# Performance work log

Hardware: AMD Instinct MI355X
Metric: run time of the kernel (lower is better)

Reference implementation:

```python
import jax, jax.numpy as jnp
import numpy as np

N = 50000      # nodes
E = 800000     # edges (before self loops)
F_IN = 16      # n_input_features
PRE = 32       # n_channels_preproc
C = 128        # n_channels
GH = 32        # edge_gate_hidden_dim
L = 5          # n_gnn_layers (tied weights)


def setup_inputs() -> dict:
    key = jax.random.key(0)
    ks = jax.random.split(key, 16)
    def w(k, shape):
        return jax.random.normal(k, shape, jnp.float32) * 0.05
    return dict(
        x=jax.random.normal(ks[0], (N, F_IN), jnp.float32),
        edge_index=jax.random.randint(ks[1], (2, E), 0, N),
        edge_attr=jax.random.normal(ks[2], (E, 1), jnp.float32),
        W_pre=w(ks[3], (F_IN, PRE)), b_pre=jnp.zeros((PRE,), jnp.float32),
        W_init=w(ks[4], (PRE, C)), b_init=jnp.zeros((C,), jnp.float32),
        W_g1=w(ks[5], (2 * C + 1, GH)), b_g1=jnp.zeros((GH,), jnp.float32),
        W_g2=w(ks[6], (GH, 1)), b_g2=jnp.zeros((1,), jnp.float32),
        W_z=w(ks[7], (2 * C, C)), b_z=jnp.zeros((C,), jnp.float32),
        W_r=w(ks[8], (2 * C, C)), b_r=jnp.zeros((C,), jnp.float32),
        W_h=w(ks[9], (2 * C, C)), b_h=jnp.zeros((C,), jnp.float32),
        W_f1=w(ks[10], (2 * C, C)), b_f1=jnp.zeros((C,), jnp.float32),
        W_f2=w(ks[11], (C, 2)), b_f2=jnp.zeros((2,), jnp.float32),
    )


def reference(x, edge_index, edge_attr,
              W_pre, b_pre, W_init, b_init,
              W_g1, b_g1, W_g2, b_g2,
              W_z, b_z, W_r, b_r, W_h, b_h,
              W_f1, b_f1, W_f2, b_f2):
    n = x.shape[0]
    # add self loops (fill_value=0.0 for edge_attr)
    sl = jnp.arange(n)
    row = jnp.concatenate([edge_index[0], sl])   # source (x_j)
    col = jnp.concatenate([edge_index[1], sl])   # target (x_i), aggregation index
    ea = jnp.concatenate([edge_attr, jnp.zeros((n, 1), x.dtype)], axis=0)
    # symmetric normalization from in-degree (degree of col, incl. self loops)
    deg = jax.ops.segment_sum(jnp.ones(col.shape[0], x.dtype), col, num_segments=n)
    dis = jnp.where(deg > 0, deg ** -0.5, 0.0)
    norm = (dis[row] * dis[col])[:, None]        # [E', 1]

    # preproc + initial node transform
    h = jax.nn.relu(x @ W_pre + b_pre)
    h0 = jax.nn.relu(h @ W_init + b_init)
    h = h0

    for _ in range(L):  # tied GGNN layers
        x_i = h[col]                              # gather target feats  [E', C]
        x_j = h[row]                              # gather source feats  [E', C]
        g_in = jnp.concatenate([x_i, x_j, ea], axis=-1)          # [E', 2C+1]
        gate = jax.nn.sigmoid(jax.nn.relu(g_in @ W_g1 + b_g1) @ W_g2 + b_g2)
        msg = gate * (norm * x_j)                                  # [E', C]
        aggr = jax.ops.segment_sum(msg, col, num_segments=n)       # scatter-add
        # GRU-style update
        za = jnp.concatenate([h, aggr], axis=-1)                   # [N, 2C]
        z = jax.nn.sigmoid(za @ W_z + b_z)
        r = jax.nn.sigmoid(za @ W_r + b_r)
        hc = jax.nn.relu(jnp.concatenate([r * h, aggr], axis=-1) @ W_h + b_h)
        h = (1.0 - z) * h + z * hc

    out = jnp.concatenate([h0, h], axis=-1)       # [N, 2C]
    out = jax.nn.relu(out @ W_f1 + b_f1)
    return out @ W_f2 + b_f2                      # [N, 2] logits (output_activation='none')
```

## Files before the change

### kernel.cpp

```cpp
#include <hip/hip_runtime.h>
#include <math.h>

#define NODES 50000
#define NEDGES 800000
#define ETOT (NEDGES + NODES)
#define FIN 16
#define PRE 32
#define C 128
#define GH 32
#define LAYERS 5
#define RECS 160
#define SCB 64
#define SCT 256
#define SCCH ((NODES + SCB*SCT - 1) / (SCB*SCT))

typedef _Float16 f16;
typedef f16 f16x8 __attribute__((ext_vector_type(8)));
typedef f16 f16x4 __attribute__((ext_vector_type(4)));
typedef f16 f16x2 __attribute__((ext_vector_type(2)));
typedef float f32x4 __attribute__((ext_vector_type(4)));

__device__ __forceinline__ float sigmoidf_(float x) { return 1.0f / (1.0f + __expf(-x)); }

__device__ __forceinline__ int swz_off(int row, int bytecol, int stride) {
    return row * stride + ((((bytecol) >> 4) ^ (row & 7)) << 4) + (bytecol & 15);
}
__device__ __forceinline__ int ps_off(int row, int bytecol) {
    return row * 64 + ((((bytecol) >> 4) ^ (row & 3)) << 4) + (bytecol & 15);
}

__device__ __forceinline__ int bperm(int c) { return 4 * (c & 7) + (c >> 3); }

__global__ void k_degree(const int* __restrict__ col, float* __restrict__ deg) {
    int e = blockIdx.x * blockDim.x + threadIdx.x;
    if (e < NEDGES) atomicAdd(&deg[col[e]], 1.0f);
}

__global__ __launch_bounds__(SCT) void k_scan1(const float* __restrict__ deg, int* __restrict__ bsum) {
    __shared__ int ws4[SCT / 64];
    int b = blockIdx.x, t = threadIdx.x;
    int lane = t & 63, wv = t >> 6;
    int base = (b * SCT + t) * SCCH;
    int sum = 0;
#pragma unroll
    for (int j = 0; j < SCCH; j++) {
        int i = base + j;
        if (i < NODES) sum += (int)deg[i] + 1;
    }
#pragma unroll
    for (int off = 32; off > 0; off >>= 1) sum += __shfl_xor(sum, off, 64);
    if (lane == 0) ws4[wv] = sum;
    __syncthreads();
    if (t == 0) {
        int tot = 0;
#pragma unroll
        for (int j = 0; j < SCT / 64; j++) tot += ws4[j];
        bsum[b] = tot;
    }
}

__global__ __launch_bounds__(64) void k_scan2(const int* __restrict__ bsum, int* __restrict__ bscan,
                                              int* __restrict__ start) {
    int t = threadIdx.x;
    int v = (t < SCB) ? bsum[t] : 0;
    int x = v;
#pragma unroll
    for (int off = 1; off < 64; off <<= 1) {
        int tt = __shfl_up(x, off, 64);
        if (t >= off) x += tt;
    }
    if (t < SCB) bscan[t] = x - v;
    if (t == SCB - 1) start[NODES] = x;
}

__global__ __launch_bounds__(SCT) void k_scan3(
    float* __restrict__ deg_dis, const int* __restrict__ bscan,
    int* __restrict__ start, int* __restrict__ cursor) {
    __shared__ int woff[SCT / 64];
    int b = blockIdx.x, t = threadIdx.x;
    int lane = t & 63, wv = t >> 6;
    int base = (b * SCT + t) * SCCH;
    int v[SCCH]; int sum = 0;
#pragma unroll
    for (int j = 0; j < SCCH; j++) {
        int i = base + j;
        v[j] = (i < NODES) ? (int)deg_dis[i] + 1 : 0;
        sum += v[j];
    }
    int x = sum;
#pragma unroll
    for (int off = 1; off < 64; off <<= 1) {
        int tt = __shfl_up(x, off, 64);
        if (lane >= off) x += tt;
    }
    int texcl = x - sum;
    if (lane == 63) woff[wv] = x;
    __syncthreads();
    int wbase = 0;
    for (int j = 0; j < wv; j++) wbase += woff[j];
    int run = bscan[b] + wbase + texcl;
#pragma unroll
    for (int j = 0; j < SCCH; j++) {
        int i = base + j;
        if (i < NODES) {
            start[i] = run; cursor[i] = run;
            deg_dis[i] = rsqrtf((float)v[j]);
        }
        run += v[j];
    }
}

__global__ __launch_bounds__(256) void k_csr(
    const int* __restrict__ eidx, const float* __restrict__ eattr,
    int* __restrict__ cursor,
    int* __restrict__ row_sorted, float* __restrict__ ea_sorted) {
    int e = blockIdx.x * blockDim.x + threadIdx.x;
    if (e >= ETOT) return;
    int r, ci; float ea;
    if (e < NEDGES) { r = eidx[e]; ci = eidx[NEDGES + e]; ea = eattr[e]; }
    else            { r = ci = e - NEDGES; ea = 0.0f; }
    int slot = atomicAdd(&cursor[ci], 1);
    row_sorted[slot] = r;
    ea_sorted[slot] = ea;
}

__global__ __launch_bounds__(256) void k_prep_w(
    const float* __restrict__ Wz, const float* __restrict__ Wr, const float* __restrict__ Wh,
    const float* __restrict__ Wg1, const float* __restrict__ Wf1,
    const float* __restrict__ Wpre, const float* __restrict__ Winit,
    f16* __restrict__ WcatF, f16* __restrict__ WhtopF, f16* __restrict__ Wg1F,
    f16* __restrict__ Wf1F, f16* __restrict__ WpreF, f16* __restrict__ WinitF) {
    int t = blockIdx.x * 256 + threadIdx.x;
    int l = t & 63;
    int lr = l & 15, lh = l >> 4;
    if (t < 24 * 8 * 64) {
        int idx = t >> 6; int nt = idx >> 3, ks = idx & 7;
        int wv = nt / 6, ntl = nt % 6;
        int grp = ntl >> 1, pr = ntl & 1;
        int ncol = (2 * wv + pr) * 16 + lr;
        f16x8 v;
#pragma unroll
        for (int j = 0; j < 8; j++) {
            int k = ks * 32 + lh * 8 + j;
            float x;
            if (grp == 0)      x = Wz[k * 128 + ncol];
            else if (grp == 1) x = Wr[k * 128 + ncol];
            else               x = (k >= 128) ? Wh[k * 128 + ncol] : 0.0f;
            v[j] = (f16)x;
        }
        *(f16x8*)(WcatF + (size_t)t * 8) = v;
    } else if (t < 24 * 8 * 64 + 8 * 4 * 64) {
        int t2 = t - 24 * 8 * 64;
        int idx = t2 >> 6; int nt = idx >> 2, ks = idx & 3;
        int n = nt * 16 + lr;
        f16x8 v;
#pragma unroll
        for (int j = 0; j < 8; j++) {
            int k = ks * 32 + lh * 8 + j;
            v[j] = (f16)Wh[k * 128 + n];
        }
        *(f16x8*)(WhtopF + (size_t)t2 * 8) = v;
    } else if (t < 24 * 8 * 64 + 8 * 4 * 64 + 4 * 4 * 64) {
        int t3 = t - (24 * 8 * 64 + 8 * 4 * 64);
        int idx = t3 >> 6; int nt = idx >> 2, ks = idx & 3;
        int cg = nt * 16 + lr;
        f16x8 v;
#pragma unroll
        for (int j = 0; j < 8; j++) {
            int k = ks * 32 + lh * 8 + j;
            v[j] = (f16)((cg < 32) ? Wg1[k * GH + cg] : Wg1[(128 + k) * GH + (cg - 32)]);
        }
        *(f16x8*)(Wg1F + (size_t)t3 * 8) = v;
    } else if (t < 24 * 8 * 64 + 8 * 4 * 64 + 4 * 4 * 64 + 8 * 8 * 64) {
        int t4 = t - (24 * 8 * 64 + 8 * 4 * 64 + 4 * 4 * 64);
        int idx = t4 >> 6; int nt = idx >> 3, ks = idx & 7;
        int n = nt * 16 + lr;
        f16x8 v;
#pragma unroll
        for (int j = 0; j < 8; j++) {
            int k = ks * 32 + lh * 8 + j;
            v[j] = (f16)Wf1[k * 128 + n];
        }
        *(f16x8*)(Wf1F + (size_t)t4 * 8) = v;
    } else if (t < 19456 + 2 * 64) {
        int t5 = t - 19456;
        int nt = t5 >> 6;
        f16x8 v;
#pragma unroll
        for (int j = 0; j < 8; j++) {
            int k = lh * 8 + j;
            v[j] = (k < FIN) ? (f16)Wpre[k * PRE + nt * 16 + lr] : (f16)0.0f;
        }
        *(f16x8*)(WpreF + (size_t)t5 * 8) = v;
    } else if (t < 19456 + 128 + 8 * 64) {
        int t6 = t - 19456 - 128;
        int nt = t6 >> 6;
        f16x8 v;
#pragma unroll
        for (int j = 0; j < 8; j++) {
            int k = lh * 8 + j;
            v[j] = (f16)Winit[k * C + nt * 16 + lr];
        }
        *(f16x8*)(WinitF + (size_t)t6 * 8) = v;
    }
}

__global__ __launch_bounds__(256) void k_pre_gate(
    const float* __restrict__ x, const float* __restrict__ bpre, const float* __restrict__ binit,
    const float* __restrict__ dis,
    const f16* __restrict__ WpreF, const f16* __restrict__ WinitF,
    const f16* __restrict__ Wg1F, const float* __restrict__ bg1,
    f16* __restrict__ h0_16, f16* __restrict__ h16, f16* __restrict__ rec,
    float* __restrict__ A) {
    __shared__ f16 ps[32 * 32];
    __shared__ f16 za[32 * 128];
    char* psB = (char*)ps;
    char* zaB = (char*)za;
    int tid = threadIdx.x;
    int l = tid & 63, w = tid >> 6;
    int lr = l & 15, lh = l >> 4;
    int n0 = blockIdx.x * 32;
    int rt0 = w >> 1, ct = w & 1;

    f16x8 xa = {};
    {
        int gn = n0 + rt0 * 16 + lr;
        if (gn < NODES && lh < 2) {
            float4 xv0 = *(const float4*)(x + (size_t)gn * FIN + lh * 8);
            float4 xv1 = *(const float4*)(x + (size_t)gn * FIN + lh * 8 + 4);
            xa[0] = (f16)xv0.x; xa[1] = (f16)xv0.y; xa[2] = (f16)xv0.z; xa[3] = (f16)xv0.w;
            xa[4] = (f16)xv1.x; xa[5] = (f16)xv1.y; xa[6] = (f16)xv1.z; xa[7] = (f16)xv1.w;
        }
    }
    f16x8 bA = *(const f16x8*)(WpreF + ((size_t)ct * 64 + l) * 8);
    f32x4 accA; accA[0] = accA[1] = accA[2] = accA[3] = 0.0f;
    accA = __builtin_amdgcn_mfma_f32_16x16x32_f16(xa, bA, accA, 0, 0, 0);
    {
        float bp = bpre[ct * 16 + lr];
#pragma unroll
        for (int j = 0; j < 4; j++) {
            int row = rt0 * 16 + lh * 4 + j;
            float v = fmaxf(accA[j] + bp, 0.0f);
            *(f16*)(psB + ps_off(row, (ct * 16 + lr) * 2)) = (f16)v;
        }
    }
    __syncthreads();

    f16x8 pa0 = *(const f16x8*)(psB + ps_off(lr, lh * 16));
    f16x8 pa1 = *(const f16x8*)(psB + ps_off(lr + 16, lh * 16));
    f32x4 accB[2][2];
#pragma unroll
    for (int rt = 0; rt < 2; rt++)
#pragma unroll
        for (int ntl = 0; ntl < 2; ntl++)
#pragma unroll
            for (int j = 0; j < 4; j++) accB[rt][ntl][j] = 0.0f;
#pragma unroll
    for (int ntl = 0; ntl < 2; ntl++) {
        f16x8 b = *(const f16x8*)(WinitF + ((size_t)((w * 2 + ntl) * 64 + l)) * 8);
        accB[0][ntl] = __builtin_amdgcn_mfma_f32_16x16x32_f16(pa0, b, accB[0][ntl], 0, 0, 0);
        accB[1][ntl] = __builtin_amdgcn_mfma_f32_16x16x32_f16(pa1, b, accB[1][ntl], 0, 0, 0);
    }
#pragma unroll
    for (int rt = 0; rt < 2; rt++)
#pragma unroll
        for (int ntl = 0; ntl < 2; ntl++) {
            int cg = (w * 2 + ntl) * 16 + lr;
            float bi = binit[cg];
#pragma unroll
            for (int j = 0; j < 4; j++) {
                int row = rt * 16 + lh * 4 + j;
                float v = fmaxf(accB[rt][ntl][j] + bi, 0.0f);
                *(f16*)(zaB + swz_off(row, cg * 2, 256)) = (f16)v;
            }
        }
    __syncthreads();

    for (int p = tid; p < 32 * 16; p += 256) {
        int row = p >> 4, seg = p & 15;
        int gn = n0 + row;
        if (gn < NODES) {
            f16x8 v = *(const f16x8*)(zaB + swz_off(row, seg * 16, 256));
            *(f16x8*)(h0_16 + (size_t)gn * C + seg * 8) = v;
            *(f16x8*)(h16 + (size_t)gn * C + seg * 8) = v;
            float dn = dis[gn];
            f16x8 od;
#pragma unroll
            for (int j = 0; j < 8; j++) od[j] = (f16)((float)v[j] * dn);
            *(f16x8*)(rec + (size_t)gn * RECS + 32 + seg * 8) = od;
        }
    }

    f32x4 acc3[2];
#pragma unroll
    for (int rt = 0; rt < 2; rt++)
#pragma unroll
        for (int j = 0; j < 4; j++) acc3[rt][j] = 0.0f;
#pragma unroll
    for (int ks = 0; ks < 4; ks++) {
        int kk = ks * 32 + lh * 8;
        f16x8 a0 = *(const f16x8*)(zaB + swz_off(lr,      kk * 2, 256));
        f16x8 a1 = *(const f16x8*)(zaB + swz_off(lr + 16, kk * 2, 256));
        f16x8 b = *(const f16x8*)(Wg1F + ((size_t)(w * 4 + ks) * 64 + l) * 8);
        acc3[0] = __builtin_amdgcn_mfma_f32_16x16x32_f16(a0, b, acc3[0], 0, 0, 0);
        acc3[1] = __builtin_amdgcn_mfma_f32_16x16x32_f16(a1, b, acc3[1], 0, 0, 0);
    }
    int col3 = w * 16 + lr;
#pragma unroll
    for (int rt = 0; rt < 2; rt++)
#pragma unroll
        for (int j = 0; j < 4; j++) {
            int row = rt * 16 + lh * 4 + j;
            int gn = n0 + row;
            if (gn < NODES) {
                float v = acc3[rt][j];
                if (col3 < 32) A[(size_t)gn * GH + bperm(col3)] = v + bg1[col3];
                else           rec[(size_t)gn * RECS + bperm(col3 - 32)] = (f16)v;
            }
        }
}

__global__ __launch_bounds__(256) void k_msg(
    const int* __restrict__ start, const int* __restrict__ row_sorted,
    const float* __restrict__ ea_sorted, const float* __restrict__ dis,
    const float* __restrict__ A, const f16* __restrict__ rec,
    const float* __restrict__ Wg1, const float* __restrict__ Wg2, const float* __restrict__ bg2,
    f16* __restrict__ aggr16) {
    int wid = (blockIdx.x * blockDim.x + threadIdx.x) >> 6;
    int lane = threadIdx.x & 63;
    if (wid >= NODES) return;
    int k8 = lane & 7;
    int q = lane >> 3;
    int s0 = start[wid], s1 = start[wid + 1];
    float4 a4 = *(const float4*)(A + (size_t)wid * GH + k8 * 4);
    const float* wg1e = Wg1 + 2 * C * GH;
    float wea0 = wg1e[k8], wea1 = wg1e[k8 + 8], wea2 = wg1e[k8 + 16], wea3 = wg1e[k8 + 24];
    float w20 = Wg2[k8], w21 = Wg2[k8 + 8], w22 = Wg2[k8 + 16], w23 = Wg2[k8 + 24];
    float b2 = bg2[0];
    float dci = dis[wid];
    float acc[16];
#pragma unroll
    for (int j = 0; j < 16; j++) acc[j] = 0.0f;

    int s = s0 + q;
    f16x8 ha0 = {}, hb0 = {};
    f16x4 bb0 = {};
    float ea0 = 0.0f;
    if (s < s1) {
        int r = row_sorted[s];
        ea0 = ea_sorted[s];
        const f16* rr = rec + (size_t)r * RECS;
        bb0 = *(const f16x4*)(rr + k8 * 4);
        ha0 = *(const f16x8*)(rr + 32 + k8 * 16);
        hb0 = *(const f16x8*)(rr + 32 + k8 * 16 + 8);
    }
    while (s < s1) {
        int s2 = s + 8;
        f16x8 ha1 = {}, hb1 = {};
        f16x4 bb1 = {};
        float ea1 = 0.0f;
        if (s2 < s1) {
            int r = row_sorted[s2];
            ea1 = ea_sorted[s2];
            const f16* rr = rec + (size_t)r * RECS;
            bb1 = *(const f16x4*)(rr + k8 * 4);
            ha1 = *(const f16x8*)(rr + 32 + k8 * 16);
            hb1 = *(const f16x8*)(rr + 32 + k8 * 16 + 8);
        }
        float t0 = fmaxf(a4.x + (float)bb0[0] + ea0 * wea0, 0.0f);
        float t1 = fmaxf(a4.y + (float)bb0[1] + ea0 * wea1, 0.0f);
        float t2 = fmaxf(a4.z + (float)bb0[2] + ea0 * wea2, 0.0f);
        float t3 = fmaxf(a4.w + (float)bb0[3] + ea0 * wea3, 0.0f);
        float p = t0 * w20;
        p = fmaf(t1, w21, p);
        p = fmaf(t2, w22, p);
        p = fmaf(t3, w23, p);
        p += __shfl_xor(p, 4, 8);
        p += __shfl_xor(p, 2, 8);
        p += __shfl_xor(p, 1, 8);
        float coef = sigmoidf_(p + b2);
#pragma unroll
        for (int j = 0; j < 8; j++) {
            acc[j]     = fmaf(coef, (float)ha0[j], acc[j]);
            acc[8 + j] = fmaf(coef, (float)hb0[j], acc[8 + j]);
        }
        ha0 = ha1; hb0 = hb1; bb0 = bb1; ea0 = ea1;
        s = s2;
    }
#pragma unroll
    for (int j = 0; j < 16; j++) {
        acc[j] += __shfl_xor(acc[j], 8, 64);
        acc[j] += __shfl_xor(acc[j], 16, 64);
        acc[j] += __shfl_xor(acc[j], 32, 64);
    }
    if (lane < 8) {
        f16x8 o1, o2;
#pragma unroll
        for (int j = 0; j < 8; j++) { o1[j] = (f16)(acc[j] * dci); o2[j] = (f16)(acc[8 + j] * dci); }
        *(f16x8*)(aggr16 + (size_t)wid * C + k8 * 16) = o1;
        *(f16x8*)(aggr16 + (size_t)wid * C + k8 * 16 + 8) = o2;
    }
}

__global__ __launch_bounds__(256) void k_update_mfma(
    f16* __restrict__ h16, const f16* __restrict__ aggr16, const float* __restrict__ dis,
    f16* __restrict__ rec,
    const f16* __restrict__ WcatF, const f16* __restrict__ WhtopF, const f16* __restrict__ Wg1F,
    const float* __restrict__ bz, const float* __restrict__ br, const float* __restrict__ bh,
    const float* __restrict__ bg1,
    float* __restrict__ A) {
    __shared__ f16 za[32 * 256];
    __shared__ f16 rhbuf[32 * 128];
    char* zaB = (char*)za;
    char* rhB = (char*)rhbuf;
    int tid = threadIdx.x;
    int l = tid & 63, w = tid >> 6;
    int lr = l & 15, lh = l >> 4;
    int n0 = blockIdx.x * 32;

    for (int p = tid; p < 32 * 16; p += 256) {
        int row = p >> 4, seg = p & 15;
        int gn = n0 + row;
        f16x8 v = {};
        if (gn < NODES) v = *(const f16x8*)(h16 + (size_t)gn * C + seg * 8);
        *(f16x8*)(zaB + swz_off(row, seg * 16, 512)) = v;
    }
    for (int p = tid; p < 32 * 16; p += 256) {
        int row = p >> 4, seg = p & 15;
        int gn = n0 + row;
        f16x8 v = {};
        if (gn < NODES) v = *(const f16x8*)(aggr16 + (size_t)gn * C + seg * 8);
        *(f16x8*)(zaB + swz_off(row, 256 + seg * 16, 512)) = v;
    }
    __syncthreads();

    f32x4 acc[2][6];
#pragma unroll
    for (int rt = 0; rt < 2; rt++)
#pragma unroll
        for (int n = 0; n < 6; n++)
#pragma unroll
            for (int j = 0; j < 4; j++) acc[rt][n][j] = 0.0f;
#pragma unroll
    for (int ks = 0; ks < 8; ks++) {
        int kk = ks * 32 + lh * 8;
        f16x8 a0 = *(const f16x8*)(zaB + swz_off(lr,      kk * 2, 512));
        f16x8 a1 = *(const f16x8*)(zaB + swz_off(lr + 16, kk * 2, 512));
#pragma unroll
        for (int ntl = 0; ntl < 6; ntl++) {
            f16x8 b = *(const f16x8*)(WcatF + ((size_t)((w * 6 + ntl) * 8 + ks) * 64 + l) * 8);
            acc[0][ntl] = __builtin_amdgcn_mfma_f32_16x16x32_f16(a0, b, acc[0][ntl], 0, 0, 0);
            acc[1][ntl] = __builtin_amdgcn_mfma_f32_16x16x32_f16(a1, b, acc[1][ntl], 0, 0, 0);
        }
    }

    float zreg[2][2][4];
#pragma unroll
    for (int rt = 0; rt < 2; rt++)
#pragma unroll
        for (int pr = 0; pr < 2; pr++) {
            int cg = (2 * w + pr) * 16 + lr;
#pragma unroll
            for (int j = 0; j < 4; j++) {
                int row = rt * 16 + lh * 4 + j;
                zreg[rt][pr][j] = sigmoidf_(acc[rt][pr][j] + bz[cg]);
                float rv = sigmoidf_(acc[rt][2 + pr][j] + br[cg]);
                float hv = (float)*(const f16*)(zaB + swz_off(row, cg * 2, 512));
                *(f16*)(rhB + swz_off(row, cg * 2, 256)) = (f16)(rv * hv);
            }
        }
    __syncthreads();

    f32x4 acc2[2][2];
#pragma unroll
    for (int rt = 0; rt < 2; rt++)
#pragma unroll
        for (int pr = 0; pr < 2; pr++) {
            int cg = (2 * w + pr) * 16 + lr;
#pragma unroll
            for (int j = 0; j < 4; j++)
                acc2[rt][pr][j] = acc[rt][4 + pr][j] + bh[cg];
        }
#pragma unroll
    for (int ks = 0; ks < 4; ks++) {
        int kk = ks * 32 + lh * 8;
        f16x8 a0 = *(const f16x8*)(rhB + swz_off(lr,      kk * 2, 256));
        f16x8 a1 = *(const f16x8*)(rhB + swz_off(lr + 16, kk * 2, 256));
#pragma unroll
        for (int pr = 0; pr < 2; pr++) {
            f16x8 b = *(const f16x8*)(WhtopF + ((size_t)((w * 2 + pr) * 4 + ks) * 64 + l) * 8);
            acc2[0][pr] = __builtin_amdgcn_mfma_f32_16x16x32_f16(a0, b, acc2[0][pr], 0, 0, 0);
            acc2[1][pr] = __builtin_amdgcn_mfma_f32_16x16x32_f16(a1, b, acc2[1][pr], 0, 0, 0);
        }
    }

#pragma unroll
    for (int rt = 0; rt < 2; rt++)
#pragma unroll
        for (int pr = 0; pr < 2; pr++) {
            int cg = (2 * w + pr) * 16 + lr;
#pragma unroll
            for (int j = 0; j < 4; j++) {
                int row = rt * 16 + lh * 4 + j;
                int gn = n0 + row;
                float hc = fmaxf(acc2[rt][pr][j], 0.0f);
                float z = zreg[rt][pr][j];
                float hold = (float)*(const f16*)(zaB + swz_off(row, cg * 2, 512));
                float hn = (1.0f - z) * hold + z * hc;
                if (gn < NODES) {
                    h16[(size_t)gn * C + cg] = (f16)hn;
                    rec[(size_t)gn * RECS + 32 + cg] = (f16)(hn * dis[gn]);
                }
                *(f16*)(zaB + swz_off(row, cg * 2, 512)) = (f16)hn;
            }
        }
    __syncthreads();

    f32x4 acc3[2];
#pragma unroll
    for (int rt = 0; rt < 2; rt++)
#pragma unroll
        for (int j = 0; j < 4; j++) acc3[rt][j] = 0.0f;
#pragma unroll
    for (int ks = 0; ks < 4; ks++) {
        int kk = ks * 32 + lh * 8;
        f16x8 a0 = *(const f16x8*)(zaB + swz_off(lr,      kk * 2, 512));
        f16x8 a1 = *(const f16x8*)(zaB + swz_off(lr + 16, kk * 2, 512));
        f16x8 b = *(const f16x8*)(Wg1F + ((size_t)(w * 4 + ks) * 64 + l) * 8);
        acc3[0] = __builtin_amdgcn_mfma_f32_16x16x32_f16(a0, b, acc3[0], 0, 0, 0);
        acc3[1] = __builtin_amdgcn_mfma_f32_16x16x32_f16(a1, b, acc3[1], 0, 0, 0);
    }
    int col3 = w * 16 + lr;
#pragma unroll
    for (int rt = 0; rt < 2; rt++)
#pragma unroll
        for (int j = 0; j < 4; j++) {
            int row = rt * 16 + lh * 4 + j;
            int gn = n0 + row;
            if (gn < NODES) {
                float v = acc3[rt][j];
                if (col3 < 32) A[(size_t)gn * GH + bperm(col3)] = v + bg1[col3];
                else           rec[(size_t)gn * RECS + bperm(col3 - 32)] = (f16)v;
            }
        }
}

__global__ __launch_bounds__(256) void k_final_mfma(
    const f16* __restrict__ h0_16, const f16* __restrict__ h16,
    const f16* __restrict__ Wf1F, const float* __restrict__ bf1,
    const float* __restrict__ Wf2, const float* __restrict__ bf2,
    float* __restrict__ out) {
    __shared__ float fs[32][132];
    char* zaB = (char*)&fs[0][0];
    int tid = threadIdx.x;
    int l = tid & 63, w = tid >> 6;
    int lr = l & 15, lh = l >> 4;
    int n0 = blockIdx.x * 32;

    for (int p = tid; p < 32 * 16; p += 256) {
        int row = p >> 4, seg = p & 15;
        int gn = n0 + row;
        f16x8 v = {};
        if (gn < NODES) v = *(const f16x8*)(h0_16 + (size_t)gn * C + seg * 8);
        *(f16x8*)(zaB + swz_off(row, seg * 16, 512)) = v;
    }
    for (int p = tid; p < 32 * 16; p += 256) {
        int row = p >> 4, seg = p & 15;
        int gn = n0 + row;
        f16x8 v = {};
        if (gn < NODES) v = *(const f16x8*)(h16 + (size_t)gn * C + seg * 8);
        *(f16x8*)(zaB + swz_off(row, 256 + seg * 16, 512)) = v;
    }
    __syncthreads();

    f32x4 acc[2][2];
#pragma unroll
    for (int rt = 0; rt < 2; rt++)
#pragma unroll
        for (int n = 0; n < 2; n++)
#pragma unroll
            for (int j = 0; j < 4; j++) acc[rt][n][j] = 0.0f;
#pragma unroll
    for (int ks = 0; ks < 8; ks++) {
        int kk = ks * 32 + lh * 8;
        f16x8 a0 = *(const f16x8*)(zaB + swz_off(lr,      kk * 2, 512));
        f16x8 a1 = *(const f16x8*)(zaB + swz_off(lr + 16, kk * 2, 512));
#pragma unroll
        for (int ntl = 0; ntl < 2; ntl++) {
            f16x8 b = *(const f16x8*)(Wf1F + ((size_t)((w * 2 + ntl) * 8 + ks) * 64 + l) * 8);
            acc[0][ntl] = __builtin_amdgcn_mfma_f32_16x16x32_f16(a0, b, acc[0][ntl], 0, 0, 0);
            acc[1][ntl] = __builtin_amdgcn_mfma_f32_16x16x32_f16(a1, b, acc[1][ntl], 0, 0, 0);
        }
    }
    __syncthreads();

#pragma unroll
    for (int rt = 0; rt < 2; rt++)
#pragma unroll
        for (int ntl = 0; ntl < 2; ntl++) {
            int cg = (w * 2 + ntl) * 16 + lr;
#pragma unroll
            for (int j = 0; j < 4; j++) {
                int row = rt * 16 + lh * 4 + j;
                fs[row][cg] = fmaxf(acc[rt][ntl][j] + bf1[cg], 0.0f);
            }
        }
    __syncthreads();

    if (tid < 64) {
        int n = tid >> 1, o = tid & 1;
        int gn = n0 + n;
        if (gn < NODES) {
            float a = bf2[o];
#pragma unroll 16
            for (int c = 0; c < C; c++) a = fmaf(fs[n][c], Wf2[c * 2 + o], a);
            out[(size_t)gn * 2 + o] = a;
        }
    }
}

extern "C" void kernel_launch(void* const* d_in, const int* in_sizes, int n_in,
                              void* d_out, int out_size, void* d_ws, size_t ws_size,
                              hipStream_t stream) {
    const float* x    = (const float*)d_in[0];
    const int*   eidx = (const int*)d_in[1];
    const float* eattr= (const float*)d_in[2];
    const float* Wpre = (const float*)d_in[3];  const float* bpre = (const float*)d_in[4];
    const float* Winit= (const float*)d_in[5];  const float* binit= (const float*)d_in[6];
    const float* Wg1  = (const float*)d_in[7];  const float* bg1  = (const float*)d_in[8];
    const float* Wg2  = (const float*)d_in[9];  const float* bg2  = (const float*)d_in[10];
    const float* Wz   = (const float*)d_in[11]; const float* bz   = (const float*)d_in[12];
    const float* Wr   = (const float*)d_in[13]; const float* br   = (const float*)d_in[14];
    const float* Wh   = (const float*)d_in[15]; const float* bh   = (const float*)d_in[16];
    const float* Wf1  = (const float*)d_in[17]; const float* bf1  = (const float*)d_in[18];
    const float* Wf2  = (const float*)d_in[19]; const float* bf2  = (const float*)d_in[20];
    float* out = (float*)d_out;

    float* ws  = (float*)d_ws;
    float* dis = ws;
    float* A   = dis + NODES;
    int*   start = (int*)(A + (size_t)NODES * GH);
    int*   cursor = start + NODES + 1;
    int*   bsum  = cursor + NODES + 1;
    int*   bscan = bsum + SCB;
    int*   row_sorted = bscan + SCB;
    float* ea_sorted  = (float*)(row_sorted + ETOT);
    size_t f16_base = (size_t)((ea_sorted + ETOT) - ws);
    f16_base = (f16_base + 3) & ~(size_t)3;
    f16* h0_16  = (f16*)(ws + f16_base);
    f16* h16    = h0_16 + (size_t)NODES * C;
    f16* rec    = h16 + (size_t)NODES * C;
    f16* aggr16 = rec + (size_t)NODES * RECS;
    f16* WcatF  = aggr16 + (size_t)NODES * C;
    f16* WhtopF = WcatF + 24 * 8 * 64 * 8;
    f16* Wg1F   = WhtopF + 8 * 4 * 64 * 8;
    f16* Wf1F   = Wg1F + 4 * 4 * 64 * 8;
    f16* WpreF  = Wf1F + 8 * 8 * 64 * 8;
    f16* WinitF = WpreF + 2 * 64 * 8;
    size_t f16_total = (size_t)NODES * (C + C + RECS + C)
                     + (24 * 8 + 8 * 4 + 4 * 4 + 8 * 8 + 2 + 8) * 64 * 8;
    const size_t REQ = (f16_base + (f16_total + 1) / 2) * sizeof(float);
    if (ws_size < REQ) return;

    hipMemsetAsync(dis, 0, NODES * sizeof(float), stream);
    k_degree<<<(NEDGES + 255) / 256, 256, 0, stream>>>(eidx + NEDGES, dis);
    k_scan1<<<SCB, SCT, 0, stream>>>(dis, bsum);
    k_scan2<<<1, 64, 0, stream>>>(bsum, bscan, start);
    k_scan3<<<SCB, SCT, 0, stream>>>(dis, bscan, start, cursor);
    k_csr<<<(ETOT + 255) / 256, 256, 0, stream>>>(eidx, eattr, cursor, row_sorted, ea_sorted);
    k_prep_w<<<(19456 + 128 + 512 + 255) / 256, 256, 0, stream>>>(
        Wz, Wr, Wh, Wg1, Wf1, Wpre, Winit, WcatF, WhtopF, Wg1F, Wf1F, WpreF, WinitF);
    k_pre_gate<<<(NODES + 31) / 32, 256, 0, stream>>>(
        x, bpre, binit, dis, WpreF, WinitF, Wg1F, bg1, h0_16, h16, rec, A);

    for (int l = 0; l < LAYERS; l++) {
        k_msg<<<(NODES * 64 + 255) / 256, 256, 0, stream>>>(
            start, row_sorted, ea_sorted, dis, A, rec, Wg1, Wg2, bg2, aggr16);
        k_update_mfma<<<(NODES + 31) / 32, 256, 0, stream>>>(
            h16, aggr16, dis, rec, WcatF, WhtopF, Wg1F, bz, br, bh, bg1, A);
    }
    k_final_mfma<<<(NODES + 31) / 32, 256, 0, stream>>>(h0_16, h16, Wf1F, bf1, Wf2, bf2, out);
}
```

Baseline: 580.1 us.

## Drop separate h16 buffer and pack sorted edge source and attribute together

After: 567.8 us. -2.1%, faster.

```diff
diff --git a/kernel.cpp b/kernel.cpp
--- a/kernel.cpp
+++ b/kernel.cpp
@@ -74,7 +74,7 @@
 }
 
 __global__ __launch_bounds__(SCT) void k_scan3(
-    float* __restrict__ deg_dis, const int* __restrict__ bscan,
+    float* __restrict__ deg_dis, float* __restrict__ rdis, const int* __restrict__ bscan,
     int* __restrict__ start, int* __restrict__ cursor) {
     __shared__ int woff[SCT / 64];
     int b = blockIdx.x, t = threadIdx.x;
@@ -104,7 +104,9 @@
         int i = base + j;
         if (i < NODES) {
             start[i] = run; cursor[i] = run;
-            deg_dis[i] = rsqrtf((float)v[j]);
+            float fv = (float)v[j];
+            deg_dis[i] = rsqrtf(fv);
+            rdis[i] = sqrtf(fv);
         }
         run += v[j];
     }
@@ -112,16 +114,14 @@
 
 __global__ __launch_bounds__(256) void k_csr(
     const int* __restrict__ eidx, const float* __restrict__ eattr,
-    int* __restrict__ cursor,
-    int* __restrict__ row_sorted, float* __restrict__ ea_sorted) {
+    int* __restrict__ cursor, int2* __restrict__ esort) {
     int e = blockIdx.x * blockDim.x + threadIdx.x;
     if (e >= ETOT) return;
     int r, ci; float ea;
     if (e < NEDGES) { r = eidx[e]; ci = eidx[NEDGES + e]; ea = eattr[e]; }
     else            { r = ci = e - NEDGES; ea = 0.0f; }
     int slot = atomicAdd(&cursor[ci], 1);
-    row_sorted[slot] = r;
-    ea_sorted[slot] = ea;
+    esort[slot] = make_int2(r, __float_as_int(ea));
 }
 
 __global__ __launch_bounds__(256) void k_prep_w(
@@ -210,7 +210,7 @@
     const float* __restrict__ dis,
     const f16* __restrict__ WpreF, const f16* __restrict__ WinitF,
     const f16* __restrict__ Wg1F, const float* __restrict__ bg1,
-    f16* __restrict__ h0_16, f16* __restrict__ h16, f16* __restrict__ rec,
+    f16* __restrict__ h0_16, f16* __restrict__ rec,
     float* __restrict__ A) {
     __shared__ f16 ps[32 * 32];
     __shared__ f16 za[32 * 128];
@@ -282,7 +282,6 @@
         if (gn < NODES) {
             f16x8 v = *(const f16x8*)(zaB + swz_off(row, seg * 16, 256));
             *(f16x8*)(h0_16 + (size_t)gn * C + seg * 8) = v;
-            *(f16x8*)(h16 + (size_t)gn * C + seg * 8) = v;
             float dn = dis[gn];
             f16x8 od;
 #pragma unroll
@@ -321,8 +320,8 @@
 }
 
 __global__ __launch_bounds__(256) void k_msg(
-    const int* __restrict__ start, const int* __restrict__ row_sorted,
-    const float* __restrict__ ea_sorted, const float* __restrict__ dis,
+    const int* __restrict__ start, const int2* __restrict__ esort,
+    const float* __restrict__ dis,
     const float* __restrict__ A, const f16* __restrict__ rec,
     const float* __restrict__ Wg1, const float* __restrict__ Wg2, const float* __restrict__ bg2,
     f16* __restrict__ aggr16) {
@@ -347,9 +346,9 @@
     f16x4 bb0 = {};
     float ea0 = 0.0f;
     if (s < s1) {
-        int r = row_sorted[s];
-        ea0 = ea_sorted[s];
-        const f16* rr = rec + (size_t)r * RECS;
+        int2 e0 = esort[s];
+        ea0 = __int_as_float(e0.y);
+        const f16* rr = rec + (size_t)e0.x * RECS;
         bb0 = *(const f16x4*)(rr + k8 * 4);
         ha0 = *(const f16x8*)(rr + 32 + k8 * 16);
         hb0 = *(const f16x8*)(rr + 32 + k8 * 16 + 8);
@@ -360,9 +359,9 @@
         f16x4 bb1 = {};
         float ea1 = 0.0f;
         if (s2 < s1) {
-            int r = row_sorted[s2];
-            ea1 = ea_sorted[s2];
-            const f16* rr = rec + (size_t)r * RECS;
+            int2 e1 = esort[s2];
+            ea1 = __int_as_float(e1.y);
+            const f16* rr = rec + (size_t)e1.x * RECS;
             bb1 = *(const f16x4*)(rr + k8 * 4);
             ha1 = *(const f16x8*)(rr + 32 + k8 * 16);
             hb1 = *(const f16x8*)(rr + 32 + k8 * 16 + 8);
@@ -403,8 +402,8 @@
 }
 
 __global__ __launch_bounds__(256) void k_update_mfma(
-    f16* __restrict__ h16, const f16* __restrict__ aggr16, const float* __restrict__ dis,
-    f16* __restrict__ rec,
+    f16* __restrict__ rec, const f16* __restrict__ aggr16,
+    const float* __restrict__ dis, const float* __restrict__ rdis,
     const f16* __restrict__ WcatF, const f16* __restrict__ WhtopF, const f16* __restrict__ Wg1F,
     const float* __restrict__ bz, const float* __restrict__ br, const float* __restrict__ bh,
     const float* __restrict__ bg1,
@@ -422,7 +421,12 @@
         int row = p >> 4, seg = p & 15;
         int gn = n0 + row;
         f16x8 v = {};
-        if (gn < NODES) v = *(const f16x8*)(h16 + (size_t)gn * C + seg * 8);
+        if (gn < NODES) {
+            v = *(const f16x8*)(rec + (size_t)gn * RECS + 32 + seg * 8);
+            float rd = rdis[gn];
+#pragma unroll
+            for (int j = 0; j < 8; j++) v[j] = (f16)((float)v[j] * rd);
+        }
         *(f16x8*)(zaB + swz_off(row, seg * 16, 512)) = v;
     }
     for (int p = tid; p < 32 * 16; p += 256) {
@@ -508,7 +512,6 @@
                 float hold = (float)*(const f16*)(zaB + swz_off(row, cg * 2, 512));
                 float hn = (1.0f - z) * hold + z * hc;
                 if (gn < NODES) {
-                    h16[(size_t)gn * C + cg] = (f16)hn;
                     rec[(size_t)gn * RECS + 32 + cg] = (f16)(hn * dis[gn]);
                 }
                 *(f16*)(zaB + swz_off(row, cg * 2, 512)) = (f16)hn;
@@ -546,7 +549,7 @@
 }
 
 __global__ __launch_bounds__(256) void k_final_mfma(
-    const f16* __restrict__ h0_16, const f16* __restrict__ h16,
+    const f16* __restrict__ h0_16, const f16* __restrict__ rec, const float* __restrict__ rdis,
     const f16* __restrict__ Wf1F, const float* __restrict__ bf1,
     const float* __restrict__ Wf2, const float* __restrict__ bf2,
     float* __restrict__ out) {
@@ -568,7 +571,12 @@
         int row = p >> 4, seg = p & 15;
         int gn = n0 + row;
         f16x8 v = {};
-        if (gn < NODES) v = *(const f16x8*)(h16 + (size_t)gn * C + seg * 8);
+        if (gn < NODES) {
+            v = *(const f16x8*)(rec + (size_t)gn * RECS + 32 + seg * 8);
+            float rd = rdis[gn];
+#pragma unroll
+            for (int j = 0; j < 8; j++) v[j] = (f16)((float)v[j] * rd);
+        }
         *(f16x8*)(zaB + swz_off(row, 256 + seg * 16, 512)) = v;
     }
     __syncthreads();
@@ -638,18 +646,17 @@
 
     float* ws  = (float*)d_ws;
     float* dis = ws;
-    float* A   = dis + NODES;
+    float* rdis= dis + NODES;
+    float* A   = rdis + NODES;
     int*   start = (int*)(A + (size_t)NODES * GH);
     int*   cursor = start + NODES + 1;
     int*   bsum  = cursor + NODES + 1;
     int*   bscan = bsum + SCB;
-    int*   row_sorted = bscan + SCB;
-    float* ea_sorted  = (float*)(row_sorted + ETOT);
-    size_t f16_base = (size_t)((ea_sorted + ETOT) - ws);
+    int2*  esort = (int2*)(bscan + SCB);
+    size_t f16_base = (size_t)((int*)(esort + ETOT) - (int*)ws);
     f16_base = (f16_base + 3) & ~(size_t)3;
     f16* h0_16  = (f16*)(ws + f16_base);
-    f16* h16    = h0_16 + (size_t)NODES * C;
-    f16* rec    = h16 + (size_t)NODES * C;
+    f16* rec    = h0_16 + (size_t)NODES * C;
     f16* aggr16 = rec + (size_t)NODES * RECS;
     f16* WcatF  = aggr16 + (size_t)NODES * C;
     f16* WhtopF = WcatF + 24 * 8 * 64 * 8;
@@ -657,7 +664,7 @@
     f16* Wf1F   = Wg1F + 4 * 4 * 64 * 8;
     f16* WpreF  = Wf1F + 8 * 8 * 64 * 8;
     f16* WinitF = WpreF + 2 * 64 * 8;
-    size_t f16_total = (size_t)NODES * (C + C + RECS + C)
+    size_t f16_total = (size_t)NODES * (C + RECS + C)
                      + (24 * 8 + 8 * 4 + 4 * 4 + 8 * 8 + 2 + 8) * 64 * 8;
     const size_t REQ = (f16_base + (f16_total + 1) / 2) * sizeof(float);
     if (ws_size < REQ) return;
@@ -666,18 +673,18 @@
     k_degree<<<(NEDGES + 255) / 256, 256, 0, stream>>>(eidx + NEDGES, dis);
     k_scan1<<<SCB, SCT, 0, stream>>>(dis, bsum);
     k_scan2<<<1, 64, 0, stream>>>(bsum, bscan, start);
-    k_scan3<<<SCB, SCT, 0, stream>>>(dis, bscan, start, cursor);
-    k_csr<<<(ETOT + 255) / 256, 256, 0, stream>>>(eidx, eattr, cursor, row_sorted, ea_sorted);
+    k_scan3<<<SCB, SCT, 0, stream>>>(dis, rdis, bscan, start, cursor);
+    k_csr<<<(ETOT + 255) / 256, 256, 0, stream>>>(eidx, eattr, cursor, esort);
     k_prep_w<<<(19456 + 128 + 512 + 255) / 256, 256, 0, stream>>>(
         Wz, Wr, Wh, Wg1, Wf1, Wpre, Winit, WcatF, WhtopF, Wg1F, Wf1F, WpreF, WinitF);
     k_pre_gate<<<(NODES + 31) / 32, 256, 0, stream>>>(
-        x, bpre, binit, dis, WpreF, WinitF, Wg1F, bg1, h0_16, h16, rec, A);
+        x, bpre, binit, dis, WpreF, WinitF, Wg1F, bg1, h0_16, rec, A);
 
     for (int l = 0; l < LAYERS; l++) {
         k_msg<<<(NODES * 64 + 255) / 256, 256, 0, stream>>>(
-            start, row_sorted, ea_sorted, dis, A, rec, Wg1, Wg2, bg2, aggr16);
+            start, esort, dis, A, rec, Wg1, Wg2, bg2, aggr16);
         k_update_mfma<<<(NODES + 31) / 32, 256, 0, stream>>>(
-            h16, aggr16, dis, rec, WcatF, WhtopF, Wg1F, bz, br, bh, bg1, A);
-    }
-    k_final_mfma<<<(NODES + 31) / 32, 256, 0, stream>>>(h0_16, h16, Wf1F, bf1, Wf2, bf2, out);
-}
+            rec, aggr16, dis, rdis, WcatF, WhtopF, Wg1F, bz, br, bh, bg1, A);
+    }
+    k_final_mfma<<<(NODES + 31) / 32, 256, 0, stream>>>(h0_16, rec, rdis, Wf1F, bf1, Wf2, bf2, out);
+}
```
